# Kernel tuning notes

Hardware: AMD Instinct MI355X
Metric: run time of the kernel (lower is better)

## Reference

```python
import jax, jax.numpy as jnp
import numpy as np

N = 50000
E = 800000
F_IN = 128
HEADS = 8
HID = 16
CLASSES = 40
NEG_SLOPE = 0.2


def setup_inputs() -> dict:
    key = jax.random.key(0)
    ks = jax.random.split(key, 10)
    return {
        "x": jax.random.normal(ks[0], (N, F_IN), jnp.float32),
        "edge_index": jax.random.randint(ks[1], (2, E), 0, N, jnp.int64),
        "W1": jax.random.normal(ks[2], (F_IN, HEADS * HID), jnp.float32) * 0.1,
        "a_src1": jax.random.normal(ks[3], (HEADS, HID), jnp.float32) * 0.1,
        "a_dst1": jax.random.normal(ks[4], (HEADS, HID), jnp.float32) * 0.1,
        "b1": jax.random.normal(ks[5], (HEADS * HID,), jnp.float32) * 0.1,
        "W2": jax.random.normal(ks[6], (HEADS * HID, CLASSES), jnp.float32) * 0.1,
        "a_src2": jax.random.normal(ks[7], (1, CLASSES), jnp.float32) * 0.1,
        "a_dst2": jax.random.normal(ks[8], (1, CLASSES), jnp.float32) * 0.1,
        "b2": jax.random.normal(ks[9], (CLASSES,), jnp.float32) * 0.1,
    }


def gat_conv(x, src, dst, W, a_src, a_dst, bias, heads, out_ch, concat):
    # x: [N, in] -> h: [N, H, C]
    h = (x @ W).reshape(N, heads, out_ch)
    e_src = jnp.einsum("nhc,hc->nh", h, a_src)  # [N, H]
    e_dst = jnp.einsum("nhc,hc->nh", h, a_dst)
    alpha = e_src[src] + e_dst[dst]             # [E, H]
    alpha = jax.nn.leaky_relu(alpha, NEG_SLOPE)
    # segment softmax over incoming edges of each dst node
    amax = jax.ops.segment_max(alpha, dst, num_segments=N)
    alpha = jnp.exp(alpha - amax[dst])
    denom = jax.ops.segment_sum(alpha, dst, num_segments=N)
    alpha = alpha / (denom[dst] + 1e-16)
    msg = h[src] * alpha[:, :, None]            # [E, H, C]
    out = jax.ops.segment_sum(msg, dst, num_segments=N)  # [N, H, C]
    out = out.reshape(N, heads * out_ch) if concat else out.mean(axis=1)
    return out + bias


def reference(x, edge_index, W1, a_src1, a_dst1, b1, W2, a_src2, a_dst2, b2):
    # PyG GATConv adds self-loops by default
    loops = jnp.arange(N, dtype=edge_index.dtype)
    src = jnp.concatenate([edge_index[0], loops])
    dst = jnp.concatenate([edge_index[1], loops])
    # inference: dropout layers are identity
    h = gat_conv(x, src, dst, W1, a_src1, a_dst1, b1, HEADS, HID, concat=True)
    h = jax.nn.elu(h)
    out = gat_conv(h, src, dst, W2, a_src2, a_dst2, b2, 1, CLASSES, concat=False)
    return out
```

## Files before the change

### kernel.cpp

```cpp
#include <hip/hip_runtime.h>
#include <math.h>

#define NN 50000
#define EE 800000
#define ET (EE + NN)
#define F_IN 128
#define HEADS 8
#define HID 16
#define C1 (HEADS * HID)
#define CLASSES 40
#define NEG_SLOPE 0.2f
#define LOG2E 1.4426950408889634f

#define NCHUNKS ((NN + 1023) / 1024)
#define NHIST 64
#define EPB (EE / NHIST)
#define PADN (NCHUNKS * 1024)
#define LDSW (PADN / 4)
#define GB ((NN + 63) / 64)
#define FSUB 5
#define FPB (EPB / FSUB)
#define FILLB (NHIST * FSUB)

typedef __attribute__((ext_vector_type(8))) short bf16x8;
typedef __attribute__((ext_vector_type(4))) float f32x4;
typedef __attribute__((ext_vector_type(8))) _Float16 h16x8;
typedef __attribute__((ext_vector_type(2))) _Float16 h16x2;

__device__ __forceinline__ unsigned cvtpk(float a, float b) {
    unsigned r;
    asm("v_cvt_pk_bf16_f32 %0, %1, %2" : "=v"(r) : "v"(a), "v"(b));
    return r;
}
__device__ __forceinline__ float fexp2(float x) {
    float r;
    asm("v_exp_f32 %0, %1\n\ts_nop 0" : "=v"(r) : "v"(x));
    return r;
}
__device__ __forceinline__ float bflo(unsigned u) { return __uint_as_float(u << 16); }
__device__ __forceinline__ float bfhi(unsigned u) { return __uint_as_float(u & 0xffff0000u); }
__device__ __forceinline__ float lrelu(float a) { return fmaxf(a, NEG_SLOPE * a); }
__device__ __forceinline__ unsigned short bf1(float a) { return (unsigned short)cvtpk(a, a); }
__device__ __forceinline__ float bf1f(float a) { return bflo(cvtpk(a, a)); }
__device__ __forceinline__ bf16x8 pack8(float f0, float f1, float f2, float f3,
                                        float f4, float f5, float f6, float f7) {
    union { unsigned u[4]; bf16x8 v; } U;
    U.u[0] = cvtpk(f0, f1);
    U.u[1] = cvtpk(f2, f3);
    U.u[2] = cvtpk(f4, f5);
    U.u[3] = cvtpk(f6, f7);
    return U.v;
}

__global__ void prep_kernel(const float* __restrict__ W1,
                            const float* __restrict__ as1, const float* __restrict__ ad1,
                            const float* __restrict__ W2,
                            const float* __restrict__ as2, const float* __restrict__ ad2,
                            const int* __restrict__ ei,
                            unsigned short* __restrict__ va1h, unsigned short* __restrict__ va1l,
                            unsigned short* __restrict__ va2b,
                            unsigned short* __restrict__ W1b, unsigned short* __restrict__ W2b,
                            unsigned char* __restrict__ partial8,
                            unsigned char* __restrict__ rank8) {
    const int tid = threadIdx.x;
    const int b = blockIdx.x;
    if (b >= 3) {
        __shared__ unsigned lhist[LDSW];
        for (int i = tid; i < LDSW; i += 256) lhist[i] = 0;
        __syncthreads();
        const int hb = b - 3;
        const int* dp = ei + EE + hb * EPB;
        unsigned char* rk = rank8 + (size_t)hb * EPB;
        for (int e0 = tid * 4; e0 < EPB; e0 += 1024) {
            int4 d4 = *(const int4*)(dp + e0);
            uchar4 r;
            {
                const unsigned d = (unsigned)d4.x, sh8 = (d & 3) << 3;
                unsigned old = atomicAdd(&lhist[d >> 2], 1u << sh8);
                r.x = (unsigned char)((old >> sh8) & 0xff);
            }
            {
                const unsigned d = (unsigned)d4.y, sh8 = (d & 3) << 3;
                unsigned old = atomicAdd(&lhist[d >> 2], 1u << sh8);
                r.y = (unsigned char)((old >> sh8) & 0xff);
            }
            {
                const unsigned d = (unsigned)d4.z, sh8 = (d & 3) << 3;
                unsigned old = atomicAdd(&lhist[d >> 2], 1u << sh8);
                r.z = (unsigned char)((old >> sh8) & 0xff);
            }
            {
                const unsigned d = (unsigned)d4.w, sh8 = (d & 3) << 3;
                unsigned old = atomicAdd(&lhist[d >> 2], 1u << sh8);
                r.w = (unsigned char)((old >> sh8) & 0xff);
            }
            *(uchar4*)(rk + e0) = r;
        }
        __syncthreads();
        unsigned* pb = (unsigned*)(partial8 + (size_t)hb * PADN);
        for (int i = tid; i < LDSW; i += 256) pb[i] = lhist[i];
        return;
    }
    if (b == 1) {
        for (int f = tid; f < 2048; f += 256) {
            const int lane = f & 63, kc = (f >> 6) & 3, ntw = f >> 8;
            const int q = lane >> 4, c = lane & 15;
            const int col = ntw * 16 + c;
            const int k0 = kc * 32 + q * 8;
            const float* wp = W1 + (size_t)k0 * C1 + col;
            *(bf16x8*)(W1b + (size_t)f * 8) =
                pack8(wp[0], wp[C1], wp[2 * C1], wp[3 * C1],
                      wp[4 * C1], wp[5 * C1], wp[6 * C1], wp[7 * C1]);
        }
        return;
    }
    if (b == 2) {
        for (int f = tid; f < 768; f += 256) {
            const int lane = f & 63, kc = (f >> 6) & 3, nt = f >> 8;
            const int q = lane >> 4, c = lane & 15;
            const int col = nt * 16 + c;
            const int k0 = kc * 32 + q * 8;
            bf16x8 v = 0;
            if (col < CLASSES) {
                const float* wp = W2 + (size_t)k0 * CLASSES + col;
                v = pack8(wp[0], wp[CLASSES], wp[2 * CLASSES], wp[3 * CLASSES],
                          wp[4 * CLASSES], wp[5 * CLASSES], wp[6 * CLASSES], wp[7 * CLASSES]);
            }
            *(bf16x8*)(W2b + (size_t)f * 8) = v;
        }
        return;
    }
    {
        const int k = tid >> 1, half = tid & 1;
        const float* wrow = W1 + (size_t)k * C1 + half * 64;
        #pragma unroll
        for (int hh = 0; hh < 4; ++hh) {
            const int h = half * 4 + hh;
            float s = 0.f, d = 0.f;
            #pragma unroll
            for (int t = 0; t < 16; ++t) {
                float wv = wrow[hh * 16 + t];
                s += wv * as1[h * HID + t];
                d += wv * ad1[h * HID + t];
            }
            s *= LOG2E; d *= LOG2E;
            va1h[h * 128 + k]       = bf1(s);
            va1l[h * 128 + k]       = bf1(s - bf1f(s));
            va1h[(h + 8) * 128 + k] = bf1(d);
            va1l[(h + 8) * 128 + k] = bf1(d - bf1f(d));
        }
    }
    if (tid < C1) {
        const float* wrow = W2 + (size_t)tid * CLASSES;
        float s = 0.f, d = 0.f;
        #pragma unroll
        for (int c2 = 0; c2 < CLASSES; ++c2) {
            float wv = wrow[c2];
            s += wv * as2[c2];
            d += wv * ad2[c2];
        }
        s *= LOG2E; d *= LOG2E;
        va2b[0 * 128 + tid] = bf1(s);
        va2b[1 * 128 + tid] = bf1(s - bf1f(s));
        va2b[2 * 128 + tid] = bf1(d);
        va2b[3 * 128 + tid] = bf1(d - bf1f(d));
    }
}

__global__ void scan1_kernel(const unsigned char* __restrict__ partial8,
                             unsigned char* __restrict__ pfx8,
                             int* __restrict__ deg,
                             int* __restrict__ rowptr, int* __restrict__ bsum) {
    __shared__ int sh[256];
    const int tid = threadIdx.x;
    const int base = blockIdx.x * 1024 + tid * 4;
    int t0 = 0, t1 = 0, t2 = 0, t3 = 0;
    #pragma unroll 8
    for (int b = 0; b < NHIST; ++b) {
        uchar4 pf;
        pf.x = (unsigned char)t0; pf.y = (unsigned char)t1;
        pf.z = (unsigned char)t2; pf.w = (unsigned char)t3;
        *(uchar4*)(pfx8 + (size_t)b * PADN + base) = pf;
        uchar4 p = *(const uchar4*)(partial8 + (size_t)b * PADN + base);
        t0 += p.x; t1 += p.y; t2 += p.z; t3 += p.w;
    }
    int v[4], s[4];
    v[0] = (base + 0 < NN) ? t0 + 1 : 0;
    v[1] = (base + 1 < NN) ? t1 + 1 : 0;
    v[2] = (base + 2 < NN) ? t2 + 1 : 0;
    v[3] = (base + 3 < NN) ? t3 + 1 : 0;
    #pragma unroll
    for (int j = 0; j < 4; ++j)
        if (base + j < NN) deg[base + j] = v[j];
    s[0] = v[0]; s[1] = s[0] + v[1]; s[2] = s[1] + v[2]; s[3] = s[2] + v[3];
    int T = s[3];
    sh[tid] = T;
    __syncthreads();
    for (int off = 1; off < 256; off <<= 1) {
        int xv = (tid >= off) ? sh[tid - off] : 0;
        __syncthreads();
        sh[tid] += xv;
        __syncthreads();
    }
    int excl = sh[tid] - T;
    #pragma unroll
    for (int j = 0; j < 4; ++j)
        if (base + j < NN) rowptr[base + j] = excl + s[j] - v[j];
    if (tid == 255) bsum[blockIdx.x] = sh[255];
}

__global__ void scan3_kernel(int* __restrict__ rowptr, const int* __restrict__ bsum,
                             unsigned short* __restrict__ csr) {
    __shared__ int ex[64];
    const int tid = threadIdx.x;
    if (tid < 64) {
        int v = (tid < NCHUNKS) ? bsum[tid] : 0;
        int s = v;
        #pragma unroll
        for (int off = 1; off < 64; off <<= 1) {
            int xv = __shfl_up(s, off);
            if (tid >= off) s += xv;
        }
        ex[tid] = s - v;
    }
    __syncthreads();
    int i = blockIdx.x * blockDim.x + tid;
    if (i >= NN) return;
    int rp = rowptr[i] + ex[i >> 10];
    rowptr[i] = rp;
    csr[rp] = (unsigned short)i;
}

__global__ __launch_bounds__(256, 4)
void gemm1_fill_kernel(const float* __restrict__ x,
                       const unsigned short* __restrict__ W1b,
                       const unsigned short* __restrict__ va1h,
                       const unsigned short* __restrict__ va1l,
                       const int* __restrict__ ei,
                       const int* __restrict__ rowptr,
                       const unsigned char* __restrict__ pfx8,
                       const unsigned char* __restrict__ rank8,
                       unsigned short* __restrict__ csr,
                       _Float16* __restrict__ h1h,
                       float* __restrict__ e_src, float* __restrict__ e_dst) {
    const int bid = blockIdx.x;
    const int tid = threadIdx.x;
    if (bid < FILLB) {
        const int part = bid / FSUB;
        const int chunkoff = (bid % FSUB) * FPB;
        const int gbase = part * EPB + chunkoff;
        const int* sp = ei + gbase;
        const int* dp = ei + EE + gbase;
        const unsigned char* pf = pfx8 + (size_t)part * PADN;
        const unsigned char* rk = rank8 + (size_t)part * EPB + chunkoff;
        for (int e0 = tid * 4; e0 < FPB; e0 += 1024) {
            int4 s4 = *(const int4*)(sp + e0);
            int4 d4 = *(const int4*)(dp + e0);
            uchar4 r = *(const uchar4*)(rk + e0);
            csr[rowptr[d4.x] + 1 + pf[d4.x] + r.x] = (unsigned short)s4.x;
            csr[rowptr[d4.y] + 1 + pf[d4.y] + r.y] = (unsigned short)s4.y;
            csr[rowptr[d4.z] + 1 + pf[d4.z] + r.z] = (unsigned short)s4.z;
            csr[rowptr[d4.w] + 1 + pf[d4.w] + r.w] = (unsigned short)s4.w;
        }
        return;
    }
    const int gemmb = bid - FILLB;
    const int w = tid >> 6, lane = tid & 63;
    const int q = lane >> 4, c = lane & 15;
    const int m0 = (gemmb * 4 + w) * 16;

    int row = m0 + c;
    if (row > NN - 1) row = NN - 1;
    bf16x8 afrag[4];
    #pragma unroll
    for (int kc = 0; kc < 4; ++kc) {
        const float* xp = x + (size_t)row * F_IN + kc * 32 + q * 8;
        float4 p0 = *(const float4*)xp;
        float4 p1 = *(const float4*)(xp + 4);
        afrag[kc] = pack8(p0.x, p0.y, p0.z, p0.w, p1.x, p1.y, p1.z, p1.w);
    }

    {
        f32x4 acce = {0.f, 0.f, 0.f, 0.f};
        #pragma unroll
        for (int kc = 0; kc < 4; ++kc) {
            const int coloff = kc * 32 + q * 8;
            bf16x8 beh = *(const bf16x8*)(va1h + c * 128 + coloff);
            bf16x8 bel = *(const bf16x8*)(va1l + c * 128 + coloff);
            acce = __builtin_amdgcn_mfma_f32_16x16x32_bf16(afrag[kc], beh, acce, 0, 0, 0);
            acce = __builtin_amdgcn_mfma_f32_16x16x32_bf16(afrag[kc], bel, acce, 0, 0, 0);
        }
        float* ep = (c < 8) ? e_src : e_dst;
        const int cc = c & 7;
        #pragma unroll
        for (int r = 0; r < 4; ++r) {
            const int ro = m0 + q * 4 + r;
            if (ro < NN) ep[(size_t)ro * HEADS + cc] = acce[r];
        }
    }

    #pragma unroll 2
    for (int nt = 0; nt < 8; ++nt) {
        bf16x8 bf0 = *(const bf16x8*)(W1b + (size_t)((nt * 4 + 0) * 64 + lane) * 8);
        bf16x8 bf1_ = *(const bf16x8*)(W1b + (size_t)((nt * 4 + 1) * 64 + lane) * 8);
        bf16x8 bf2 = *(const bf16x8*)(W1b + (size_t)((nt * 4 + 2) * 64 + lane) * 8);
        bf16x8 bf3 = *(const bf16x8*)(W1b + (size_t)((nt * 4 + 3) * 64 + lane) * 8);
        f32x4 a = {0.f, 0.f, 0.f, 0.f};
        a = __builtin_amdgcn_mfma_f32_16x16x32_bf16(afrag[0], bf0, a, 0, 0, 0);
        a = __builtin_amdgcn_mfma_f32_16x16x32_bf16(afrag[1], bf1_, a, 0, 0, 0);
        a = __builtin_amdgcn_mfma_f32_16x16x32_bf16(afrag[2], bf2, a, 0, 0, 0);
        a = __builtin_amdgcn_mfma_f32_16x16x32_bf16(afrag[3], bf3, a, 0, 0, 0);
        #pragma unroll
        for (int r = 0; r < 4; ++r) {
            const int ro = m0 + q * 4 + r;
            if (ro < NN) h1h[(size_t)ro * C1 + nt * 16 + c] = (_Float16)a[r];
        }
    }
}

__global__ __launch_bounds__(256)
void agg1_gemm2_kernel(const _Float16* __restrict__ h1h,
                       const float* __restrict__ e_src, const float* __restrict__ e_dst,
                       const int* __restrict__ rowptr, const int* __restrict__ deg,
                       const unsigned short* __restrict__ csr,
                       const float* __restrict__ b1,
                       const unsigned short* __restrict__ W2b,
                       const unsigned short* __restrict__ va2b,
                       _Float16* __restrict__ h2h,
                       float* __restrict__ e_src2, float* __restrict__ e_dst2) {
    __shared__ unsigned short hm[16][132];
    const int tid = threadIdx.x;
    const int grp = tid >> 4;
    const int l = tid & 15;
    const int d = blockIdx.x * 16 + grp;
    const int hd = l >> 1;
    const float ed = e_dst[(size_t)d * HEADS + hd];
    const int start = rowptr[d];
    const int cnt = deg[d];

    float denom = 0.f;
    float acc[8] = {0.f, 0.f, 0.f, 0.f, 0.f, 0.f, 0.f, 0.f};

    for (int i = 0; i < cnt; i += 8) {
        int s[8];
        #pragma unroll
        for (int e = 0; e < 8; ++e)
            s[e] = csr[start + ((i + e < cnt) ? i + e : i)];
        float es[8];
        #pragma unroll
        for (int e = 0; e < 8; ++e)
            es[e] = e_src[(size_t)s[e] * HEADS + hd];
        h16x8 g[8];
        #pragma unroll
        for (int e = 0; e < 8; ++e)
            g[e] = *(const h16x8*)(h1h + (size_t)s[e] * C1 + 8 * l);
        float w[8];
        #pragma unroll
        for (int e = 0; e < 8; ++e) {
            float we = fexp2(lrelu(es[e] + ed));
            w[e] = (i + e < cnt) ? we : 0.f;
            denom += w[e];
        }
        #pragma unroll
        for (int e = 0; e < 8; ++e) {
            #pragma unroll
            for (int j = 0; j < 8; ++j)
                acc[j] = fmaf((float)g[e][j], w[e], acc[j]);
        }
    }
    const float inv = 1.f / (denom + 1e-16f);
    float o[8];
    #pragma unroll
    for (int k = 0; k < 8; ++k) {
        float t = acc[k] * inv + b1[8 * l + k];
        o[k] = (t > 0.f) ? t : fexp2(t * LOG2E) - 1.f;
    }
    uint4 st;
    st.x = cvtpk(o[0], o[1]);
    st.y = cvtpk(o[2], o[3]);
    st.z = cvtpk(o[4], o[5]);
    st.w = cvtpk(o[6], o[7]);
    *(uint4*)(&hm[grp][8 * l]) = st;
    __syncthreads();

    if (tid < 64) {
        const int lane = tid, q = lane >> 4, c = lane & 15;
        const int m0 = blockIdx.x * 16;
        bf16x8 afrag[4];
        #pragma unroll
        for (int kc = 0; kc < 4; ++kc)
            afrag[kc] = *(const bf16x8*)(&hm[c][kc * 32 + q * 8]);

        bf16x8 bfrag[3][4];
        #pragma unroll
        for (int nt = 0; nt < 3; ++nt)
            #pragma unroll
            for (int kc = 0; kc < 4; ++kc)
                bfrag[nt][kc] = *(const bf16x8*)(W2b + (size_t)((nt * 4 + kc) * 64 + lane) * 8);
        bf16x8 bfe[4];
        #pragma unroll
        for (int kc = 0; kc < 4; ++kc) {
            bf16x8 bb = 0;
            if (c < 4) bb = *(const bf16x8*)(va2b + c * 128 + kc * 32 + q * 8);
            bfe[kc] = bb;
        }

        f32x4 a2[3] = {{0.f,0.f,0.f,0.f},{0.f,0.f,0.f,0.f},{0.f,0.f,0.f,0.f}};
        f32x4 acce = {0.f, 0.f, 0.f, 0.f};
        #pragma unroll
        for (int kc = 0; kc < 4; ++kc) {
            a2[0] = __builtin_amdgcn_mfma_f32_16x16x32_bf16(afrag[kc], bfrag[0][kc], a2[0], 0, 0, 0);
            a2[1] = __builtin_amdgcn_mfma_f32_16x16x32_bf16(afrag[kc], bfrag[1][kc], a2[1], 0, 0, 0);
            a2[2] = __builtin_amdgcn_mfma_f32_16x16x32_bf16(afrag[kc], bfrag[2][kc], a2[2], 0, 0, 0);
            acce  = __builtin_amdgcn_mfma_f32_16x16x32_bf16(afrag[kc], bfe[kc],      acce,  0, 0, 0);
        }
        #pragma unroll
        for (int r = 0; r < 4; ++r) {
            const int ro = m0 + q * 4 + r;
            float v = acce[r] + __shfl_xor(acce[r], 1);
            #pragma unroll
            for (int nt = 0; nt < 3; ++nt) {
                const int col = nt * 16 + c;
                if (col < CLASSES)
                    h2h[(size_t)ro * CLASSES + col] = (_Float16)a2[nt][r];
            }
            if (c == 0) e_src2[ro] = v;
            if (c == 2) e_dst2[ro] = v;
        }
    }
}

__global__ __launch_bounds__(64)
void agg2_kernel(const _Float16* __restrict__ h2h,
                 const float* __restrict__ e_src, const float* __restrict__ e_dst,
                 const int* __restrict__ rowptr, const int* __restrict__ deg,
                 const unsigned short* __restrict__ csr,
                 const float* __restrict__ b2, float* __restrict__ out) {
    const int tid = threadIdx.x;
    const int eg = tid / 20;
    const int c  = tid % 20;
    const int d = blockIdx.x * 3 + eg;
    const bool live = (eg < 3) && (d < NN);
    const int dcl = live ? d : 0;
    const float ed = e_dst[dcl];
    const int start = rowptr[dcl];
    const int cnt = live ? deg[dcl] : 0;

    float denom = 0.f, acc0 = 0.f, acc1 = 0.f;
    for (int i = 0; i < cnt; i += 8) {
        int s[8];
        #pragma unroll
        for (int e = 0; e < 8; ++e)
            s[e] = csr[start + ((i + e < cnt) ? i + e : i)];
        float es[8];
        #pragma unroll
        for (int e = 0; e < 8; ++e)
            es[e] = e_src[s[e]];
        h16x2 g[8];
        #pragma unroll
        for (int e = 0; e < 8; ++e)
            g[e] = *(const h16x2*)(h2h + (size_t)s[e] * CLASSES + 2 * c);
        float w[8];
        #pragma unroll
        for (int e = 0; e < 8; ++e) {
            float we = fexp2(lrelu(es[e] + ed));
            w[e] = (i + e < cnt) ? we : 0.f;
            denom += w[e];
        }
        #pragma unroll
        for (int e = 0; e < 8; ++e) {
            acc0 = fmaf((float)g[e][0], w[e], acc0);
            acc1 = fmaf((float)g[e][1], w[e], acc1);
        }
    }
    if (live) {
        const float inv = 1.f / (denom + 1e-16f);
        float2 o;
        o.x = acc0 * inv + b2[2 * c];
        o.y = acc1 * inv + b2[2 * c + 1];
        *(float2*)(out + (size_t)d * CLASSES + 2 * c) = o;
    }
}

extern "C" void kernel_launch(void* const* d_in, const int* in_sizes, int n_in,
                              void* d_out, int out_size, void* d_ws, size_t ws_size,
                              hipStream_t stream) {
    const float* x      = (const float*)d_in[0];
    const int*   ei     = (const int*)d_in[1];
    const float* W1     = (const float*)d_in[2];
    const float* a_src1 = (const float*)d_in[3];
    const float* a_dst1 = (const float*)d_in[4];
    const float* b1     = (const float*)d_in[5];
    const float* W2     = (const float*)d_in[6];
    const float* a_src2 = (const float*)d_in[7];
    const float* a_dst2 = (const float*)d_in[8];
    const float* b2     = (const float*)d_in[9];
    float* out = (float*)d_out;

    char* ws = (char*)d_ws;
    size_t off = 0;
    auto alloc = [&](size_t bytes) { char* p = ws + off; off += (bytes + 255) & ~(size_t)255; return p; };
    _Float16* h1h = (_Float16*)alloc((size_t)NN * C1 * 2);
    _Float16* h2h = (_Float16*)alloc((size_t)NN * CLASSES * 2);
    float* e_src1 = (float*)alloc((size_t)NN * HEADS * 4);
    float* e_dst1 = (float*)alloc((size_t)NN * HEADS * 4);
    float* e_src2 = (float*)alloc((size_t)NN * 4);
    float* e_dst2 = (float*)alloc((size_t)NN * 4);
    int*   deg    = (int*)alloc((size_t)NN * 4);
    int*   rowptr = (int*)alloc((size_t)NN * 4);
    unsigned short* csr  = (unsigned short*)alloc((size_t)ET * 2);
    int*   bsum   = (int*)alloc(256 * 4);
    unsigned short* va1h = (unsigned short*)alloc(16 * 128 * 2);
    unsigned short* va1l = (unsigned short*)alloc(16 * 128 * 2);
    unsigned short* va2b = (unsigned short*)alloc(4 * 128 * 2);
    unsigned short* W1b  = (unsigned short*)alloc(2048 * 8 * 2);
    unsigned short* W2b  = (unsigned short*)alloc(768 * 8 * 2);
    unsigned char* partial8 = (unsigned char*)alloc((size_t)NHIST * PADN);
    unsigned char* pfx8     = (unsigned char*)alloc((size_t)NHIST * PADN);
    unsigned char* rank8    = (unsigned char*)alloc((size_t)EE);

    prep_kernel<<<3 + NHIST, 256, 0, stream>>>(W1, a_src1, a_dst1, W2, a_src2, a_dst2, ei,
                                               va1h, va1l, va2b, W1b, W2b, partial8, rank8);
    scan1_kernel<<<NCHUNKS, 256, 0, stream>>>(partial8, pfx8, deg, rowptr, bsum);
    scan3_kernel<<<(NN + 255) / 256, 256, 0, stream>>>(rowptr, bsum, csr);
    gemm1_fill_kernel<<<FILLB + GB, 256, 0, stream>>>(x, W1b, va1h, va1l, ei, rowptr, pfx8,
                                                      rank8, csr, h1h, e_src1, e_dst1);

    agg1_gemm2_kernel<<<NN / 16, 256, 0, stream>>>(h1h, e_src1, e_dst1, rowptr, deg, csr, b1,
                                                   W2b, va2b, h2h, e_src2, e_dst2);

    agg2_kernel<<<(NN + 2) / 3, 64, 0, stream>>>(h2h, e_src2, e_dst2, rowptr, deg, csr, b2, out);
}
```

Baseline: 196.0 us.

## Fold scan3 into fill kernel, raise histogram partitions, aggregate two nodes per thread

Removes the separate scan3 launch by having every fill block recompute the block-sum prefix in shared memory and add it on the fly. Extra blocks in the fill/gemm1 kernel write the final rowptr into a separate buffer. Raises the histogram partition count from 64 to 160, shrinking per-partition edge chunks. Makes agg1_gemm2 process 32 destination nodes per block, two per thread-group, interleaving their gathers for more memory-level parallelism at the cost of extra registers and padded work for unequal degrees.

```diff
diff --git a/kernel.cpp b/kernel.cpp
--- a/kernel.cpp
+++ b/kernel.cpp
@@ -13,7 +13,7 @@
 #define LOG2E 1.4426950408889634f
 
 #define NCHUNKS ((NN + 1023) / 1024)
-#define NHIST 64
+#define NHIST 160
 #define EPB (EE / NHIST)
 #define PADN (NCHUNKS * 1024)
 #define LDSW (PADN / 4)
@@ -21,6 +21,7 @@
 #define FSUB 5
 #define FPB (EPB / FSUB)
 #define FILLB (NHIST * FSUB)
+#define S3B ((NN + 255) / 256)
 
 typedef __attribute__((ext_vector_type(8))) short bf16x8;
 typedef __attribute__((ext_vector_type(4))) float f32x4;
@@ -170,7 +171,7 @@
 __global__ void scan1_kernel(const unsigned char* __restrict__ partial8,
                              unsigned char* __restrict__ pfx8,
                              int* __restrict__ deg,
-                             int* __restrict__ rowptr, int* __restrict__ bsum) {
+                             int* __restrict__ rowptrA, int* __restrict__ bsum) {
     __shared__ int sh[256];
     const int tid = threadIdx.x;
     const int base = blockIdx.x * 1024 + tid * 4;
@@ -205,30 +206,8 @@
     int excl = sh[tid] - T;
     #pragma unroll
     for (int j = 0; j < 4; ++j)
-        if (base + j < NN) rowptr[base + j] = excl + s[j] - v[j];
+        if (base + j < NN) rowptrA[base + j] = excl + s[j] - v[j];
     if (tid == 255) bsum[blockIdx.x] = sh[255];
-}
-
-__global__ void scan3_kernel(int* __restrict__ rowptr, const int* __restrict__ bsum,
-                             unsigned short* __restrict__ csr) {
-    __shared__ int ex[64];
-    const int tid = threadIdx.x;
-    if (tid < 64) {
-        int v = (tid < NCHUNKS) ? bsum[tid] : 0;
-        int s = v;
-        #pragma unroll
-        for (int off = 1; off < 64; off <<= 1) {
-            int xv = __shfl_up(s, off);
-            if (tid >= off) s += xv;
-        }
-        ex[tid] = s - v;
-    }
-    __syncthreads();
-    int i = blockIdx.x * blockDim.x + tid;
-    if (i >= NN) return;
-    int rp = rowptr[i] + ex[i >> 10];
-    rowptr[i] = rp;
-    csr[rp] = (unsigned short)i;
 }
 
 __global__ __launch_bounds__(256, 4)
@@ -237,34 +216,57 @@
                        const unsigned short* __restrict__ va1h,
                        const unsigned short* __restrict__ va1l,
                        const int* __restrict__ ei,
-                       const int* __restrict__ rowptr,
+                       const int* __restrict__ rowptrA,
+                       const int* __restrict__ bsum,
                        const unsigned char* __restrict__ pfx8,
                        const unsigned char* __restrict__ rank8,
+                       int* __restrict__ rowptrF,
                        unsigned short* __restrict__ csr,
                        _Float16* __restrict__ h1h,
                        float* __restrict__ e_src, float* __restrict__ e_dst) {
     const int bid = blockIdx.x;
     const int tid = threadIdx.x;
-    if (bid < FILLB) {
-        const int part = bid / FSUB;
-        const int chunkoff = (bid % FSUB) * FPB;
-        const int gbase = part * EPB + chunkoff;
-        const int* sp = ei + gbase;
-        const int* dp = ei + EE + gbase;
-        const unsigned char* pf = pfx8 + (size_t)part * PADN;
-        const unsigned char* rk = rank8 + (size_t)part * EPB + chunkoff;
-        for (int e0 = tid * 4; e0 < FPB; e0 += 1024) {
-            int4 s4 = *(const int4*)(sp + e0);
-            int4 d4 = *(const int4*)(dp + e0);
-            uchar4 r = *(const uchar4*)(rk + e0);
-            csr[rowptr[d4.x] + 1 + pf[d4.x] + r.x] = (unsigned short)s4.x;
-            csr[rowptr[d4.y] + 1 + pf[d4.y] + r.y] = (unsigned short)s4.y;
-            csr[rowptr[d4.z] + 1 + pf[d4.z] + r.z] = (unsigned short)s4.z;
-            csr[rowptr[d4.w] + 1 + pf[d4.w] + r.w] = (unsigned short)s4.w;
+    if (bid < FILLB + S3B) {
+        __shared__ int ex[64];
+        if (tid < 64) {
+            int v = (tid < NCHUNKS) ? bsum[tid] : 0;
+            int s = v;
+            #pragma unroll
+            for (int off = 1; off < 64; off <<= 1) {
+                int xv = __shfl_up(s, off);
+                if (tid >= off) s += xv;
+            }
+            ex[tid] = s - v;
+        }
+        __syncthreads();
+        if (bid < FILLB) {
+            const int part = bid / FSUB;
+            const int chunkoff = (bid % FSUB) * FPB;
+            const int gbase = part * EPB + chunkoff;
+            const int* sp = ei + gbase;
+            const int* dp = ei + EE + gbase;
+            const unsigned char* pf = pfx8 + (size_t)part * PADN;
+            const unsigned char* rk = rank8 + (size_t)part * EPB + chunkoff;
+            for (int e0 = tid * 4; e0 < FPB; e0 += 1024) {
+                int4 s4 = *(const int4*)(sp + e0);
+                int4 d4 = *(const int4*)(dp + e0);
+                uchar4 r = *(const uchar4*)(rk + e0);
+                csr[rowptrA[d4.x] + ex[d4.x >> 10] + 1 + pf[d4.x] + r.x] = (unsigned short)s4.x;
+                csr[rowptrA[d4.y] + ex[d4.y >> 10] + 1 + pf[d4.y] + r.y] = (unsigned short)s4.y;
+                csr[rowptrA[d4.z] + ex[d4.z >> 10] + 1 + pf[d4.z] + r.z] = (unsigned short)s4.z;
+                csr[rowptrA[d4.w] + ex[d4.w >> 10] + 1 + pf[d4.w] + r.w] = (unsigned short)s4.w;
+            }
+        } else {
+            int i = (bid - FILLB) * 256 + tid;
+            if (i < NN) {
+                int rp = rowptrA[i] + ex[i >> 10];
+                rowptrF[i] = rp;
+                csr[rp] = (unsigned short)i;
+            }
         }
         return;
     }
-    const int gemmb = bid - FILLB;
+    const int gemmb = bid - FILLB - S3B;
     const int w = tid >> 6, lane = tid & 63;
     const int q = lane >> 4, c = lane & 15;
     const int m0 = (gemmb * 4 + w) * 16;
@@ -328,68 +330,99 @@
                        const unsigned short* __restrict__ va2b,
                        _Float16* __restrict__ h2h,
                        float* __restrict__ e_src2, float* __restrict__ e_dst2) {
-    __shared__ unsigned short hm[16][132];
+    __shared__ unsigned short hm[32][132];
     const int tid = threadIdx.x;
     const int grp = tid >> 4;
     const int l = tid & 15;
-    const int d = blockIdx.x * 16 + grp;
     const int hd = l >> 1;
-    const float ed = e_dst[(size_t)d * HEADS + hd];
-    const int start = rowptr[d];
-    const int cnt = deg[d];
-
-    float denom = 0.f;
-    float acc[8] = {0.f, 0.f, 0.f, 0.f, 0.f, 0.f, 0.f, 0.f};
-
-    for (int i = 0; i < cnt; i += 8) {
-        int s[8];
-        #pragma unroll
-        for (int e = 0; e < 8; ++e)
-            s[e] = csr[start + ((i + e < cnt) ? i + e : i)];
-        float es[8];
-        #pragma unroll
-        for (int e = 0; e < 8; ++e)
-            es[e] = e_src[(size_t)s[e] * HEADS + hd];
-        h16x8 g[8];
-        #pragma unroll
-        for (int e = 0; e < 8; ++e)
-            g[e] = *(const h16x8*)(h1h + (size_t)s[e] * C1 + 8 * l);
-        float w[8];
-        #pragma unroll
-        for (int e = 0; e < 8; ++e) {
-            float we = fexp2(lrelu(es[e] + ed));
-            w[e] = (i + e < cnt) ? we : 0.f;
-            denom += w[e];
+    const int d0 = blockIdx.x * 32 + grp;
+    const int d1t = d0 + 16;
+    const bool live1 = d1t < NN;
+    const int d1 = live1 ? d1t : d0;
+    const float ed0 = e_dst[(size_t)d0 * HEADS + hd];
+    const float ed1 = e_dst[(size_t)d1 * HEADS + hd];
+    const int st0 = rowptr[d0], st1 = rowptr[d1];
+    const int c0 = deg[d0], c1 = deg[d1];
+    const int cmax = (c0 > c1) ? c0 : c1;
+
+    float den0 = 0.f, den1 = 0.f;
+    float a0[8] = {0.f, 0.f, 0.f, 0.f, 0.f, 0.f, 0.f, 0.f};
+    float a1[8] = {0.f, 0.f, 0.f, 0.f, 0.f, 0.f, 0.f, 0.f};
+
+    for (int i = 0; i < cmax; i += 8) {
+        int s0[8], s1[8];
+        #pragma unroll
+        for (int e = 0; e < 8; ++e) {
+            s0[e] = csr[st0 + ((i + e < c0) ? i + e : c0 - 1)];
+            s1[e] = csr[st1 + ((i + e < c1) ? i + e : c1 - 1)];
+        }
+        float es0[8], es1[8];
+        #pragma unroll
+        for (int e = 0; e < 8; ++e) {
+            es0[e] = e_src[(size_t)s0[e] * HEADS + hd];
+            es1[e] = e_src[(size_t)s1[e] * HEADS + hd];
+        }
+        h16x8 g0[8], g1[8];
+        #pragma unroll
+        for (int e = 0; e < 8; ++e) {
+            g0[e] = *(const h16x8*)(h1h + (size_t)s0[e] * C1 + 8 * l);
+            g1[e] = *(const h16x8*)(h1h + (size_t)s1[e] * C1 + 8 * l);
+        }
+        float w0[8], w1[8];
+        #pragma unroll
+        for (int e = 0; e < 8; ++e) {
+            float t0 = fexp2(lrelu(es0[e] + ed0));
+            float t1 = fexp2(lrelu(es1[e] + ed1));
+            w0[e] = (i + e < c0) ? t0 : 0.f;
+            w1[e] = (i + e < c1) ? t1 : 0.f;
+            den0 += w0[e];
+            den1 += w1[e];
         }
         #pragma unroll
         for (int e = 0; e < 8; ++e) {
             #pragma unroll
-            for (int j = 0; j < 8; ++j)
-                acc[j] = fmaf((float)g[e][j], w[e], acc[j]);
-        }
-    }
-    const float inv = 1.f / (denom + 1e-16f);
-    float o[8];
-    #pragma unroll
-    for (int k = 0; k < 8; ++k) {
-        float t = acc[k] * inv + b1[8 * l + k];
-        o[k] = (t > 0.f) ? t : fexp2(t * LOG2E) - 1.f;
-    }
-    uint4 st;
-    st.x = cvtpk(o[0], o[1]);
-    st.y = cvtpk(o[2], o[3]);
-    st.z = cvtpk(o[4], o[5]);
-    st.w = cvtpk(o[6], o[7]);
-    *(uint4*)(&hm[grp][8 * l]) = st;
+            for (int j = 0; j < 8; ++j) {
+                a0[j] = fmaf((float)g0[e][j], w0[e], a0[j]);
+                a1[j] = fmaf((float)g1[e][j], w1[e], a1[j]);
+            }
+        }
+    }
+    {
+        const float inv = 1.f / (den0 + 1e-16f);
+        float o[8];
+        #pragma unroll
+        for (int k = 0; k < 8; ++k) {
+            float t = a0[k] * inv + b1[8 * l + k];
+            o[k] = (t > 0.f) ? t : fexp2(t * LOG2E) - 1.f;
+        }
+        uint4 st;
+        st.x = cvtpk(o[0], o[1]); st.y = cvtpk(o[2], o[3]);
+        st.z = cvtpk(o[4], o[5]); st.w = cvtpk(o[6], o[7]);
+        *(uint4*)(&hm[grp][8 * l]) = st;
+    }
+    {
+        const float inv = 1.f / (den1 + 1e-16f);
+        float o[8];
+        #pragma unroll
+        for (int k = 0; k < 8; ++k) {
+            float t = a1[k] * inv + b1[8 * l + k];
+            o[k] = (t > 0.f) ? t : fexp2(t * LOG2E) - 1.f;
+        }
+        uint4 st;
+        st.x = cvtpk(o[0], o[1]); st.y = cvtpk(o[2], o[3]);
+        st.z = cvtpk(o[4], o[5]); st.w = cvtpk(o[6], o[7]);
+        *(uint4*)(&hm[grp + 16][8 * l]) = st;
+    }
     __syncthreads();
 
-    if (tid < 64) {
-        const int lane = tid, q = lane >> 4, c = lane & 15;
-        const int m0 = blockIdx.x * 16;
+    if (tid < 128) {
+        const int wv = tid >> 6;
+        const int lane = tid & 63, q = lane >> 4, c = lane & 15;
+        const int m0 = blockIdx.x * 32 + wv * 16;
         bf16x8 afrag[4];
         #pragma unroll
         for (int kc = 0; kc < 4; ++kc)
-            afrag[kc] = *(const bf16x8*)(&hm[c][kc * 32 + q * 8]);
+            afrag[kc] = *(const bf16x8*)(&hm[wv * 16 + c][kc * 32 + q * 8]);
 
         bf16x8 bfrag[3][4];
         #pragma unroll
@@ -418,14 +451,16 @@
         for (int r = 0; r < 4; ++r) {
             const int ro = m0 + q * 4 + r;
             float v = acce[r] + __shfl_xor(acce[r], 1);
-            #pragma unroll
-            for (int nt = 0; nt < 3; ++nt) {
-                const int col = nt * 16 + c;
-                if (col < CLASSES)
-                    h2h[(size_t)ro * CLASSES + col] = (_Float16)a2[nt][r];
-            }
-            if (c == 0) e_src2[ro] = v;
-            if (c == 2) e_dst2[ro] = v;
+            if (ro < NN) {
+                #pragma unroll
+                for (int nt = 0; nt < 3; ++nt) {
+                    const int col = nt * 16 + c;
+                    if (col < CLASSES)
+                        h2h[(size_t)ro * CLASSES + col] = (_Float16)a2[nt][r];
+                }
+                if (c == 0) e_src2[ro] = v;
+                if (c == 2) e_dst2[ro] = v;
+            }
         }
     }
 }
@@ -506,8 +541,9 @@
     float* e_dst1 = (float*)alloc((size_t)NN * HEADS * 4);
     float* e_src2 = (float*)alloc((size_t)NN * 4);
     float* e_dst2 = (float*)alloc((size_t)NN * 4);
-    int*   deg    = (int*)alloc((size_t)NN * 4);
-    int*   rowptr = (int*)alloc((size_t)NN * 4);
+    int*   deg     = (int*)alloc((size_t)NN * 4);
+    int*   rowptrA = (int*)alloc((size_t)NN * 4);
+    int*   rowptrF = (int*)alloc((size_t)NN * 4);
     unsigned short* csr  = (unsigned short*)alloc((size_t)ET * 2);
     int*   bsum   = (int*)alloc(256 * 4);
     unsigned short* va1h = (unsigned short*)alloc(16 * 128 * 2);
@@ -521,13 +557,14 @@
 
     prep_kernel<<<3 + NHIST, 256, 0, stream>>>(W1, a_src1, a_dst1, W2, a_src2, a_dst2, ei,
                                                va1h, va1l, va2b, W1b, W2b, partial8, rank8);
-    scan1_kernel<<<NCHUNKS, 256, 0, stream>>>(partial8, pfx8, deg, rowptr, bsum);
-    scan3_kernel<<<(NN + 255) / 256, 256, 0, stream>>>(rowptr, bsum, csr);
-    gemm1_fill_kernel<<<FILLB + GB, 256, 0, stream>>>(x, W1b, va1h, va1l, ei, rowptr, pfx8,
-                                                      rank8, csr, h1h, e_src1, e_dst1);
-
-    agg1_gemm2_kernel<<<NN / 16, 256, 0, stream>>>(h1h, e_src1, e_dst1, rowptr, deg, csr, b1,
-                                                   W2b, va2b, h2h, e_src2, e_dst2);
-
-    agg2_kernel<<<(NN + 2) / 3, 64, 0, stream>>>(h2h, e_src2, e_dst2, rowptr, deg, csr, b2, out);
-}
+    scan1_kernel<<<NCHUNKS, 256, 0, stream>>>(partial8, pfx8, deg, rowptrA, bsum);
+    gemm1_fill_kernel<<<FILLB + S3B + GB, 256, 0, stream>>>(x, W1b, va1h, va1l, ei,
+                                                            rowptrA, bsum, pfx8, rank8,
+                                                            rowptrF, csr, h1h, e_src1, e_dst1);
+
+    agg1_gemm2_kernel<<<(NN + 31) / 32, 256, 0, stream>>>(h1h, e_src1, e_dst1, rowptrF, deg,
+                                                          csr, b1, W2b, va2b,
+                                                          h2h, e_src2, e_dst2);
+
+    agg2_kernel<<<(NN + 2) / 3, 64, 0, stream>>>(h2h, e_src2, e_dst2, rowptrF, deg, csr, b2, out);
+}
```

Result: no change. 194.8 us, median of 2 (-0.6%).
